# Kernel tuning notes

Measured on AMD Instinct MI355X. Metric: run time of the kernel, lower is better.

Reference implementation:

```python
import jax, jax.numpy as jnp
import numpy as np

PI = 3.141592653
PC_RANGE = np.array([-140.8, -40.0, -3.0, 140.8, 40.0, 1.0], np.float32)
IOU_THR = 0.1


def limit_period(val, offset=0.5, period=2 * PI):
    return val - jnp.floor(val / period + offset) * period


def pairwise_iou3d(boxes):
    # Axis-aligned 3D IoU approximation of the external boxes_iou3d_gpu CUDA kernel
    # (kernel source not provided). boxes: [N,7] = x,y,z,h,w,l,yaw; extents x<-l, y<-w, z<-h.
    c = boxes[:, :3]
    d = boxes[:, jnp.array([5, 4, 3])]
    lo = c - d * 0.5
    hi = c + d * 0.5
    inter = jnp.clip(jnp.minimum(hi[:, None, :], hi[None, :, :]) - jnp.maximum(lo[:, None, :], lo[None, :, :]), 0.0)
    inter_v = inter.prod(-1)                       # [N,N]
    vol = d.prod(-1)                               # [N]
    return inter_v / jnp.maximum(vol[:, None] + vol[None, :] - inter_v, 1e-8)


def cluster_assign(iou):
    # Greedy sequential clustering: repeatedly take the first unassigned box and
    # assign every box with iou > 0.1 (including already-assigned ones -> overwrite)
    # to a new cluster id. Equivalent to the original while-loop since an index,
    # once nonzero, never returns to zero, so the "first zero" scans left-to-right.
    iou = jax.lax.stop_gradient(iou)
    n = iou.shape[0]

    def body(i, carry):
        idx, cid = carry
        is_new = idx[i] == 0
        idx = jnp.where(is_new & (iou[i] > IOU_THR), cid, idx)
        return idx, cid + jnp.where(is_new, 1, 0).astype(jnp.int32)

    idx0 = jnp.zeros(n, jnp.int32)
    idx, cid = jax.lax.fori_loop(0, n, body, (idx0, jnp.int32(1)))
    return idx, cid


def cluster_fusion(boxes, scores, indices):
    n = boxes.shape[0]
    ids = jnp.arange(1, n + 1, dtype=jnp.int32)
    M = indices[None, :] == ids[:, None]            # [K,N] membership, K==N (padded)
    s_m = jnp.where(M, scores[None, :], 0.0)        # masked scores
    s_sum = s_m.sum(1)
    s_norm = s_m / jnp.maximum(s_sum, 1e-12)[:, None]
    dirs = boxes[:, 6]
    ref_idx = jnp.argmax(jnp.where(M, scores[None, :], -jnp.inf), axis=1)
    ref_dir = dirs[ref_idx]                         # yaw of max-score box per cluster
    diff = jnp.abs(dirs[None, :] - ref_dir[:, None])
    diff = jnp.where(diff > PI, 2 * PI - diff, diff)
    gt = diff > PI / 2
    score_gt = (s_m * gt).sum(1)
    score_le = s_sum - score_gt
    flip = jnp.where((score_gt <= score_le)[:, None], gt, ~gt)
    dirs_adj = limit_period(dirs[None, :] + PI * flip)
    theta = jnp.arctan2((jnp.sin(dirs_adj) * s_norm).sum(1), (jnp.cos(dirs_adj) * s_norm).sum(1))
    center_dim = s_norm @ boxes[:, :6]              # [K,6] score-weighted fusion
    boxes_fused = jnp.concatenate([center_dim, theta[:, None]], axis=1)
    # score fusion: sum_i s_sorted[i] ** (i+1), clipped to 1 (zeros from padding contribute 0)
    s_sorted = jnp.sort(s_m, axis=1)[:, ::-1]
    powers = jnp.arange(1, n + 1, dtype=jnp.float32)
    s_fused = jnp.minimum((s_sorted ** powers[None, :]).sum(1), 1.0)
    member = M.any(1)
    return boxes_fused, s_fused, member


def boxes_to_corners_3d(boxes):
    # order 'hwl': dims = h,w,l; l along x, w along y, h along z; rotate about z by yaw
    x, y, z = boxes[:, 0], boxes[:, 1], boxes[:, 2]
    h, w, l = boxes[:, 3], boxes[:, 4], boxes[:, 5]
    yaw = boxes[:, 6]
    xs = jnp.array([1, 1, -1, -1, 1, 1, -1, -1], jnp.float32) * 0.5
    ys = jnp.array([-1, 1, 1, -1, -1, 1, 1, -1], jnp.float32) * 0.5
    zs = jnp.array([-1, -1, -1, -1, 1, 1, 1, 1], jnp.float32) * 0.5
    cx = l[:, None] * xs
    cy = w[:, None] * ys
    cz = h[:, None] * zs
    c_, s_ = jnp.cos(yaw)[:, None], jnp.sin(yaw)[:, None]
    rx = cx * c_ - cy * s_
    ry = cx * s_ + cy * c_
    return jnp.stack([rx + x[:, None], ry + y[:, None], cz + z[:, None]], axis=-1)  # [N,8,3]


def setup_inputs() -> dict:
    key = jax.random.key(0)
    k1, k2, k3, k4, k5, k6 = jax.random.split(key, 6)
    C, M = 512, 8                # 512 objects seen by 8 agents -> 4096 detections
    N = C * M
    cx = jax.random.uniform(k1, (C,), minval=-120.0, maxval=120.0)
    cy = jax.random.uniform(k2, (C,), minval=-35.0, maxval=35.0)
    centers = jnp.stack([cx, cy, jnp.zeros(C)], -1)                     # [C,3]
    pos = (centers[:, None, :] + jax.random.normal(k3, (C, M, 3)) * 0.3).reshape(N, 3)
    dims = jnp.array([[1.56, 1.84, 4.2]]) + jax.random.normal(k4, (N, 3)) * 0.05  # h,w,l
    base_yaw = jax.random.uniform(k5, (C, 1), minval=-PI, maxval=PI)
    yaw = (base_yaw + jax.random.normal(k6, (C, M)) * 0.1).reshape(N, 1)
    boxes = jnp.concatenate([pos, dims, yaw], axis=1).astype(jnp.float32)
    scores = jax.random.uniform(jax.random.fold_in(key, 9), (N,), minval=0.05, maxval=0.95).astype(jnp.float32)
    return {"boxes": boxes, "scores": scores}


def reference(boxes, scores):
    boxes = boxes.at[:, 6].set(limit_period(boxes[:, 6]))
    iou = pairwise_iou3d(boxes)
    indices, _ = cluster_assign(iou)
    boxes_f, scores_f, member = cluster_fusion(boxes, scores, indices)
    corners = boxes_to_corners_3d(boxes_f)
    in_range = ((corners[..., 0] > PC_RANGE[0]) & (corners[..., 0] < PC_RANGE[3]) &
                (corners[..., 1] > PC_RANGE[1]) & (corners[..., 1] < PC_RANGE[4])).all(1)
    valid = member & in_range
    newid = jnp.cumsum(valid.astype(jnp.int32))     # remap surviving cluster ids to 1..K'
    safe = jnp.maximum(indices - 1, 0)
    new_indices = jnp.where((indices > 0) & valid[safe], newid[safe], 0)
    boxes_out = jnp.where(valid[:, None], boxes_f, 0.0)
    scores_out = jnp.where(valid, scores_f, 0.0)
    return boxes_out, scores_out, valid, new_indices
```

## Files before the change

### kernel.cpp

```cpp
#include <hip/hip_runtime.h>
#include <math.h>

#define PI_F      3.141592653f
#define TWO_PI_F  6.283185306f
#define HALF_PI_F 1.5707963265f
#define IOU_THR_F 0.1f

typedef unsigned long long u64;

__device__ __forceinline__ float limit_period_f(float v) {
    return v - floorf(v / TWO_PI_F + 0.5f) * TWO_PI_F;
}

__global__ void adj_kernel(const float* __restrict__ boxes,
                           u64* __restrict__ adjC,
                           unsigned char* __restrict__ occByte,
                           int n, int words) {
    __shared__ float jS[7][64];
    int w = blockIdx.x;
    int tid = threadIdx.x;
    int lane = tid & 63, wv = tid >> 6;
    if (tid < 64) {
        int j = (w << 6) + tid;
        if (j < n) {
            float b0 = boxes[j*7+0], b1 = boxes[j*7+1], b2 = boxes[j*7+2];
            float b3 = boxes[j*7+3], b4 = boxes[j*7+4], b5 = boxes[j*7+5];
            jS[0][tid] = b0 - b5*0.5f;  jS[3][tid] = b0 + b5*0.5f;
            jS[1][tid] = b1 - b4*0.5f;  jS[4][tid] = b1 + b4*0.5f;
            jS[2][tid] = b2 - b3*0.5f;  jS[5][tid] = b2 + b3*0.5f;
            jS[6][tid] = (b5*b4)*b3;
        }
    }
    __syncthreads();
    int i = blockIdx.y * 256 + tid;
    u64 word = 0ull;
    if (i < n) {
        float b0 = boxes[i*7+0], b1 = boxes[i*7+1], b2 = boxes[i*7+2];
        float b3 = boxes[i*7+3], b4 = boxes[i*7+4], b5 = boxes[i*7+5];
        float lix = b0 - b5*0.5f, hix = b0 + b5*0.5f;
        float liy = b1 - b4*0.5f, hiy = b1 + b4*0.5f;
        float liz = b2 - b3*0.5f, hiz = b2 + b3*0.5f;
        float vi  = (b5*b4)*b3;
        int jmax = n - (w << 6); if (jmax > 64) jmax = 64;
        for (int jj = 0; jj < jmax; ++jj) {
            float ix = fminf(hix, jS[3][jj]) - fmaxf(lix, jS[0][jj]); ix = fmaxf(ix, 0.0f);
            float iy = fminf(hiy, jS[4][jj]) - fmaxf(liy, jS[1][jj]); iy = fmaxf(iy, 0.0f);
            float iz = fminf(hiz, jS[5][jj]) - fmaxf(liz, jS[2][jj]); iz = fmaxf(iz, 0.0f);
            float inter = (ix*iy)*iz;
            float u = fmaxf(vi + jS[6][jj] - inter, 1e-8f);
            bool pred = (inter / u) > IOU_THR_F;
            word |= ((u64)(pred ? 1 : 0)) << jj;
        }
        adjC[(size_t)w * n + i] = word;
    }
    u64 bal = __ballot((i < n) && word != 0ull);
    int rb = blockIdx.y * 4 + wv;
    if (lane == 0 && rb < 64)
        occByte[rb * 64 + w] = bal ? (unsigned char)1 : (unsigned char)0;
}

__global__ __launch_bounds__(1024) void mis_node_kernel(
        const u64* __restrict__ adjC,
        const unsigned char* __restrict__ occByte,
        int* __restrict__ indices,
        int* __restrict__ seedList,
        int* __restrict__ nclust,
        int n, int words) {
    __shared__ u64 S_l[64], R_l[64], occL[64];
    __shared__ int unresolved;
    __shared__ int wsS[64];
    int tid = threadIdx.x;
    int lane = tid & 63, wv = tid >> 6;

    for (int rb = wv; rb < 64; rb += 16) {
        unsigned char b = occByte[rb * 64 + lane];
        u64 m = __ballot(b != 0);
        if (lane == 0) occL[rb] = m;
    }
    if (tid < 64) {
        int base = tid << 6;
        int vb = n - base;
        u64 valid = (vb >= 64) ? ~0ull : ((vb <= 0) ? 0ull : ((1ull << vb) - 1ull));
        S_l[tid] = 0ull;
        R_l[tid] = ~valid;
    }
    __syncthreads();

    u64 nzm[4];
    #pragma unroll
    for (int k = 0; k < 4; ++k) {
        int i = (k << 10) + tid;
        u64 nz = 0ull;
        if (i < n) {
            u64 oc = occL[i >> 6];
            while (oc) {
                int e = (int)__ffsll(oc) - 1; oc &= oc - 1;
                if (e < words && adjC[(size_t)e * n + i] != 0ull) nz |= 1ull << e;
            }
        }
        nzm[k] = nz;
    }

    unsigned done = 0;
    #pragma unroll
    for (int k = 0; k < 4; ++k)
        if (((k << 10) + tid) >= n) done |= 1u << k;

    for (;;) {
        if (tid == 0) unresolved = 0;
        unsigned pendSeed = 0, pendRes = 0;
        #pragma unroll
        for (int k = 0; k < 4; ++k) {
            if (done & (1u << k)) continue;
            int i = (k << 10) + tid;
            int w_i = i >> 6, b_i = i & 63;
            u64 sA = 0ull, uA = 0ull;
            u64 m = nzm[k];
            while (m) {
                int e = (int)__ffsll(m) - 1; m &= m - 1;
                if (e > w_i) break;
                u64 row = adjC[(size_t)e * n + i];
                u64 em = (e < w_i) ? ~0ull : (b_i ? ((1ull << b_i) - 1ull) : 0ull);
                sA |= row & S_l[e] & em;
                uA |= row & ~R_l[e] & em;
            }
            if (sA) pendRes |= 1u << k;
            else if (!uA) { pendSeed |= 1u << k; pendRes |= 1u << k; }
        }
        __syncthreads();
        #pragma unroll
        for (int k = 0; k < 4; ++k) {
            u64 bS = __ballot((pendSeed >> k) & 1u);
            u64 bR = __ballot((pendRes  >> k) & 1u);
            int w_i = ((k << 10) + tid) >> 6;
            if (lane == 0 && w_i < 64) {
                if (bS) atomicOr(&S_l[w_i], bS);
                if (bR) atomicOr(&R_l[w_i], bR);
            }
        }
        done |= pendRes;
        if ((done & 0xFu) != 0xFu) unresolved = 1;
        __syncthreads();
        if (unresolved == 0) break;
    }

    if (tid < 64) {
        int pc = (int)__popcll(S_l[tid]);
        int x = pc;
        for (int o = 1; o < 64; o <<= 1) {
            int y = __shfl_up(x, o);
            if (tid >= o) x += y;
        }
        wsS[tid] = x - pc;
        if (tid == 63) *nclust = x;
    }
    __syncthreads();
    #pragma unroll
    for (int k = 0; k < 4; ++k) {
        int i = (k << 10) + tid;
        if (i >= n) continue;
        int best = -1;
        u64 m = nzm[k];
        while (m) {
            int e = (int)__ffsll(m) - 1; m &= m - 1;
            u64 s = adjC[(size_t)e * n + i] & S_l[e];
            if (s) best = (e << 6) + 63 - (int)__clzll(s);
        }
        int idx = 0;
        if (best >= 0) {
            int w2 = best >> 6, b = best & 63;
            u64 incl = (b >= 63) ? ~0ull : ((2ull << b) - 1ull);
            idx = wsS[w2] + (int)__popcll(S_l[w2] & incl);
        }
        indices[i] = idx;
        int wj = i >> 6, bj = i & 63;
        if ((S_l[wj] >> bj) & 1ull) {
            int rank = wsS[wj] + (int)__popcll(S_l[wj] & (bj ? ((1ull << bj) - 1ull) : 0ull)) + 1;
            seedList[rank - 1] = i;
        }
    }
}

__global__ void fusion_kernel(const float* __restrict__ boxes,
                              const float* __restrict__ scores,
                              const int* __restrict__ indices,
                              const int* __restrict__ seedListG,
                              const int* __restrict__ nclust,
                              const u64* __restrict__ adjC,
                              float* __restrict__ fused,
                              float* __restrict__ sfused,
                              int* __restrict__ validArr, int n, int words) {
    int lane = threadIdx.x;
    int nc = *nclust;
    __shared__ unsigned short js[256];
    __shared__ float ms[256];
    __shared__ float ds[256];
    __shared__ float bx[6][256];
    __shared__ float sv[256], cv[256], pw[256];
    __shared__ float refdirS, denomS;
    __shared__ int   flipS, mS;
    for (int i = blockIdx.x; i < n; i += gridDim.x) {
        int cid = i + 1;
        if (cid > nc) {
            if (lane < 7) fused[i*7+lane] = 0.0f;
            if (lane == 0) { sfused[i] = 0.0f; validArr[i] = 0; }
            continue;
        }
        int s = seedListG[i];
        u64 bits = (lane < words) ? adjC[(size_t)lane * n + s] : 0ull;
        u64 keep = 0ull;
        u64 t = bits;
        while (t) {
            int b = (int)__ffsll(t) - 1;
            t &= t - 1;
            int node = (lane << 6) + b;
            if (indices[node] == cid) keep |= (1ull << b);
        }
        int cnt = __popcll(keep);
        int x = cnt;
        for (int o = 1; o < 64; o <<= 1) {
            int y = __shfl_up(x, o);
            if (lane >= o) x += y;
        }
        int excl = x - cnt;
        int m = __shfl(x, 63);
        int pos = excl;
        t = keep;
        while (t) {
            int b = (int)__ffsll(t) - 1;
            t &= t - 1;
            js[pos++] = (unsigned short)((lane << 6) + b);
        }
        __syncthreads();
        for (int k = lane; k < m; k += 64) {
            int j = js[k];
            ms[k] = scores[j];
            ds[k] = limit_period_f(boxes[j*7+6]);
            bx[0][k] = boxes[j*7+0];
            bx[1][k] = boxes[j*7+1];
            bx[2][k] = boxes[j*7+2];
            bx[3][k] = boxes[j*7+3];
            bx[4][k] = boxes[j*7+4];
            bx[5][k] = boxes[j*7+5];
        }
        __syncthreads();
        if (m == 0) {
            if (lane == 0) {
                for (int k = 0; k < 7; ++k) fused[i*7+k] = 0.0f;
                sfused[i] = 0.0f; validArr[i] = 0;
            }
            __syncthreads();
            continue;
        }
        if (lane == 0) {
            float ssum = 0.0f, smax = -1e30f; int kref = 0;
            for (int k = 0; k < m; ++k) {
                float sc = ms[k];
                ssum += sc;
                if (sc > smax) { smax = sc; kref = k; }
            }
            float refdir = ds[kref];
            float denom = fmaxf(ssum, 1e-12f);
            float sgt = 0.0f;
            for (int k = 0; k < m; ++k) {
                float d = fabsf(ds[k] - refdir);
                if (d > PI_F) d = TWO_PI_F - d;
                if (d > HALF_PI_F) sgt += ms[k];
            }
            float sle = ssum - sgt;
            refdirS = refdir; denomS = denom;
            flipS = (sgt <= sle) ? 1 : 0;
        }
        __syncthreads();
        {
            float refdir = refdirS, denom = denomS;
            bool flipGt = flipS != 0;
            for (int k = lane; k < m; k += 64) {
                float dj = ds[k];
                float d = fabsf(dj - refdir);
                if (d > PI_F) d = TWO_PI_F - d;
                bool gt = d > HALF_PI_F;
                bool flip = flipGt ? gt : !gt;
                float adj_d = limit_period_f(dj + (flip ? PI_F : 0.0f));
                float wgt = ms[k] / denom;
                sv[k] = sinf(adj_d) * wgt;
                cv[k] = cosf(adj_d) * wgt;
            }
        }
        __syncthreads();
        if (lane == 0) {
            float refdir = refdirS, denom = denomS;
            float sgt_dummy = 0.0f; (void)sgt_dummy; (void)refdir;
            float cd0=0,cd1=0,cd2=0,cd3=0,cd4=0,cd5=0;
            for (int k = 0; k < m; ++k) {
                float wgt = ms[k] / denom;
                cd0 += wgt * bx[0][k];
                cd1 += wgt * bx[1][k];
                cd2 += wgt * bx[2][k];
                cd3 += wgt * bx[3][k];
                cd4 += wgt * bx[4][k];
                cd5 += wgt * bx[5][k];
            }
            float ssin = 0.0f, scos = 0.0f;
            for (int k = 0; k < m; ++k) { ssin += sv[k]; scos += cv[k]; }
            float theta = atan2f(ssin, scos);
            for (int k = 1; k < m; ++k) {
                float key = ms[k]; int p = k - 1;
                while (p >= 0 && ms[p] < key) { ms[p+1] = ms[p]; --p; }
                ms[p+1] = key;
            }
            bx[0][255] = cd0; bx[1][255] = cd1; bx[2][255] = cd2;
            bx[3][255] = cd3; bx[4][255] = cd4; bx[5][255] = cd5;
            sv[255] = theta;
            mS = m;
        }
        __syncthreads();
        for (int k = lane; k < m; k += 64)
            pw[k] = powf(ms[k], (float)(k+1));
        __syncthreads();
        if (lane == 0) {
            float cd0 = bx[0][255], cd1 = bx[1][255], cd2 = bx[2][255];
            float cd3 = bx[3][255], cd4 = bx[4][255], cd5 = bx[5][255];
            float theta = sv[255];
            float sf = 0.0f;
            for (int k = 0; k < m; ++k) sf += pw[k];
            sf = fminf(sf, 1.0f);
            float c_ = cosf(theta), s_ = sinf(theta);
            float wdim = cd4, ldim = cd5;
            const float xs[4]  = {0.5f, 0.5f, -0.5f, -0.5f};
            const float ys_[4] = {-0.5f, 0.5f, 0.5f, -0.5f};
            bool inr = true;
            for (int c = 0; c < 4; ++c) {
                float cx = ldim * xs[c], cy = wdim * ys_[c];
                float rx = cx*c_ - cy*s_ + cd0;
                float ry = cx*s_ + cy*c_ + cd1;
                inr = inr && (rx > -140.8f) && (rx < 140.8f) && (ry > -40.0f) && (ry < 40.0f);
            }
            fused[i*7+0]=cd0; fused[i*7+1]=cd1; fused[i*7+2]=cd2;
            fused[i*7+3]=cd3; fused[i*7+4]=cd4; fused[i*7+5]=cd5;
            fused[i*7+6]=theta;
            sfused[i] = sf;
            validArr[i] = inr ? 1 : 0;
        }
        __syncthreads();
    }
}

__global__ void finalize_kernel(const float* __restrict__ fused,
                                const float* __restrict__ sfused,
                                const int* __restrict__ validArr,
                                const int* __restrict__ indices,
                                float* __restrict__ out, int n) {
    __shared__ int newidS[4096];
    __shared__ unsigned char validS[4096];
    __shared__ int scanBuf[1024];
    int tid = threadIdx.x;
    int per = (n + 1023) >> 10;
    int base = tid * per;
    int v[8];
    int sum = 0;
    for (int k = 0; k < per && k < 8; ++k) {
        int j = base + k;
        int vv = (j < n) ? validArr[j] : 0;
        v[k] = vv; sum += vv;
    }
    scanBuf[tid] = sum;
    __syncthreads();
    for (int o = 1; o < 1024; o <<= 1) {
        int val = scanBuf[tid];
        int add = (tid >= o) ? scanBuf[tid - o] : 0;
        __syncthreads();
        scanBuf[tid] = val + add;
        __syncthreads();
    }
    int run = scanBuf[tid] - sum;
    for (int k = 0; k < per && k < 8; ++k) {
        int j = base + k;
        if (j < n) { run += v[k]; newidS[j] = run; validS[j] = (unsigned char)v[k]; }
    }
    __syncthreads();
    float* boxesO  = out;
    float* scoresO = out + (size_t)7*n;
    float* validO  = out + (size_t)8*n;
    float* idxO    = out + (size_t)9*n;
    for (int j = tid; j < n; j += 1024) {
        int vv = validS[j];
        #pragma unroll
        for (int k = 0; k < 7; ++k)
            boxesO[j*7+k] = vv ? fused[j*7+k] : 0.0f;
        scoresO[j] = vv ? sfused[j] : 0.0f;
        validO[j]  = vv ? 1.0f : 0.0f;
        int ind = indices[j];
        int safe = ind - 1; if (safe < 0) safe = 0;
        bool nv = (ind > 0) && (validS[safe] != 0);
        idxO[j] = nv ? (float)newidS[safe] : 0.0f;
    }
}

extern "C" void kernel_launch(void* const* d_in, const int* in_sizes, int n_in,
                              void* d_out, int out_size, void* d_ws, size_t ws_size,
                              hipStream_t stream) {
    const float* boxes  = (const float*)d_in[0];
    const float* scores = (const float*)d_in[1];
    int n = in_sizes[0] / 7;
    int words = (n + 63) >> 6;

    char* ws = (char*)d_ws;
    size_t off = 0;
    u64* adjC = (u64*)(ws + off);
    off += (size_t)n * words * sizeof(u64);
    unsigned char* occByte = (unsigned char*)(ws + off); off += 64 * 64;
    int* seedList = (int*)(ws + off); off += (size_t)n * sizeof(int);
    int* indices  = (int*)(ws + off); off += (size_t)n * sizeof(int);
    float* fused  = (float*)(ws + off); off += (size_t)n * 7 * sizeof(float);
    float* sfused = (float*)(ws + off); off += (size_t)n * sizeof(float);
    int* validArr = (int*)(ws + off); off += (size_t)n * sizeof(int);
    int* nclust   = (int*)(ws + off); off += sizeof(int);

    dim3 adjGrid(words, (n + 255) / 256);
    adj_kernel<<<adjGrid, 256, 0, stream>>>(boxes, adjC, occByte, n, words);
    mis_node_kernel<<<1, 1024, 0, stream>>>(adjC, occByte, indices, seedList,
                                            nclust, n, words);
    fusion_kernel<<<512, 64, 0, stream>>>(boxes, scores, indices, seedList, nclust,
                                          adjC, fused, sfused, validArr, n, words);
    finalize_kernel<<<1, 1024, 0, stream>>>(fused, sfused, validArr, indices,
                                            (float*)d_out, n);
}
```

Measured before the change: 94.51 us.

## Cache neighbor rows in registers and move index assignment into fusion kernel

The single-block MIS kernel now caches up to four nonzero lower-triangle adjacency words per node in registers, with an overflow mask for the rest. This avoids reloading them from global memory on every resolution round. Thread-to-node mapping changes so each wave covers one 64-node row block. The per-node cluster index assignment moves out of the serial one-block kernel into the 512-block fusion kernel, which computes indices only for candidate members of each seed. Indices are zero-initialized in the adjacency kernel, and the seed list is built per word by scanning bits. The trade-off is more register pressure, capped 320-candidate buffers that could truncate large clusters, and redundant per-cluster index computation.

```diff
diff --git a/kernel.cpp b/kernel.cpp
--- a/kernel.cpp
+++ b/kernel.cpp
@@ -15,11 +15,16 @@
 __global__ void adj_kernel(const float* __restrict__ boxes,
                            u64* __restrict__ adjC,
                            unsigned char* __restrict__ occByte,
+                           int* __restrict__ indices,
                            int n, int words) {
     __shared__ float jS[7][64];
     int w = blockIdx.x;
     int tid = threadIdx.x;
     int lane = tid & 63, wv = tid >> 6;
+    if (blockIdx.x == 0) {
+        int i2 = blockIdx.y * 256 + tid;
+        if (i2 < n) indices[i2] = 0;
+    }
     if (tid < 64) {
         int j = (w << 6) + tid;
         if (j < n) {
@@ -59,12 +64,11 @@
         occByte[rb * 64 + w] = bal ? (unsigned char)1 : (unsigned char)0;
 }
 
-__global__ __launch_bounds__(1024) void mis_node_kernel(
+__global__ __launch_bounds__(1024) void mis_round_kernel(
         const u64* __restrict__ adjC,
         const unsigned char* __restrict__ occByte,
-        int* __restrict__ indices,
-        int* __restrict__ seedList,
-        int* __restrict__ nclust,
+        u64* __restrict__ SG, u64* __restrict__ occLG,
+        int* __restrict__ seedList, int* __restrict__ nclust,
         int n, int words) {
     __shared__ u64 S_l[64], R_l[64], occL[64];
     __shared__ int unresolved;
@@ -85,26 +89,40 @@
         R_l[tid] = ~valid;
     }
     __syncthreads();
-
-    u64 nzm[4];
+    if (tid < 64) occLG[tid] = occL[tid];
+
+    int id0[4], id1[4], id2[4], id3[4];
+    u64 r0[4], r1[4], r2[4], r3[4], rstR[4];
     #pragma unroll
     for (int k = 0; k < 4; ++k) {
-        int i = (k << 10) + tid;
-        u64 nz = 0ull;
-        if (i < n) {
-            u64 oc = occL[i >> 6];
-            while (oc) {
-                int e = (int)__ffsll(oc) - 1; oc &= oc - 1;
-                if (e < words && adjC[(size_t)e * n + i] != 0ull) nz |= 1ull << e;
-            }
-        }
-        nzm[k] = nz;
+        int rb = (k << 4) + wv;
+        int i = (rb << 6) + lane;
+        id0[k] = id1[k] = id2[k] = id3[k] = 0xFF;
+        r0[k] = r1[k] = r2[k] = r3[k] = 0ull; rstR[k] = 0ull;
+        u64 lowm = lane ? ((1ull << lane) - 1ull) : 0ull;
+        u64 oc = occL[rb] & ((rb >= 63) ? ~0ull : ((2ull << rb) - 1ull));
+        int cnt = 0;
+        while (oc) {
+            int e = (int)__ffsll(oc) - 1; oc &= oc - 1;
+            if (e >= words) break;
+            u64 row = (i < n) ? adjC[(size_t)e * n + i] : 0ull;
+            u64 em = (e < rb) ? ~0ull : lowm;
+            u64 re = row & em;
+            if (re) {
+                if      (cnt == 0) { id0[k] = e; r0[k] = re; }
+                else if (cnt == 1) { id1[k] = e; r1[k] = re; }
+                else if (cnt == 2) { id2[k] = e; r2[k] = re; }
+                else if (cnt == 3) { id3[k] = e; r3[k] = re; }
+                else rstR[k] |= 1ull << e;
+                ++cnt;
+            }
+        }
     }
 
     unsigned done = 0;
     #pragma unroll
     for (int k = 0; k < 4; ++k)
-        if (((k << 10) + tid) >= n) done |= 1u << k;
+        if ((((k << 4) + wv) << 6) + lane >= n) done |= 1u << k;
 
     for (;;) {
         if (tid == 0) unresolved = 0;
@@ -112,15 +130,19 @@
         #pragma unroll
         for (int k = 0; k < 4; ++k) {
             if (done & (1u << k)) continue;
-            int i = (k << 10) + tid;
-            int w_i = i >> 6, b_i = i & 63;
+            int rb = (k << 4) + wv;
+            int i = (rb << 6) + lane;
+            u64 lowm = lane ? ((1ull << lane) - 1ull) : 0ull;
             u64 sA = 0ull, uA = 0ull;
-            u64 m = nzm[k];
-            while (m) {
-                int e = (int)__ffsll(m) - 1; m &= m - 1;
-                if (e > w_i) break;
+            if (id0[k] != 0xFF) { sA |= r0[k] & S_l[id0[k]]; uA |= r0[k] & ~R_l[id0[k]]; }
+            if (id1[k] != 0xFF) { sA |= r1[k] & S_l[id1[k]]; uA |= r1[k] & ~R_l[id1[k]]; }
+            if (id2[k] != 0xFF) { sA |= r2[k] & S_l[id2[k]]; uA |= r2[k] & ~R_l[id2[k]]; }
+            if (id3[k] != 0xFF) { sA |= r3[k] & S_l[id3[k]]; uA |= r3[k] & ~R_l[id3[k]]; }
+            u64 rm = rstR[k];
+            while (rm) {
+                int e = (int)__ffsll(rm) - 1; rm &= rm - 1;
                 u64 row = adjC[(size_t)e * n + i];
-                u64 em = (e < w_i) ? ~0ull : (b_i ? ((1ull << b_i) - 1ull) : 0ull);
+                u64 em = (e < rb) ? ~0ull : lowm;
                 sA |= row & S_l[e] & em;
                 uA |= row & ~R_l[e] & em;
             }
@@ -132,10 +154,10 @@
         for (int k = 0; k < 4; ++k) {
             u64 bS = __ballot((pendSeed >> k) & 1u);
             u64 bR = __ballot((pendRes  >> k) & 1u);
-            int w_i = ((k << 10) + tid) >> 6;
-            if (lane == 0 && w_i < 64) {
-                if (bS) atomicOr(&S_l[w_i], bS);
-                if (bR) atomicOr(&R_l[w_i], bR);
+            int rb = (k << 4) + wv;
+            if (lane == 0 && rb < 64) {
+                if (bS) atomicOr(&S_l[rb], bS);
+                if (bR) atomicOr(&R_l[rb], bR);
             }
         }
         done |= pendRes;
@@ -145,7 +167,9 @@
     }
 
     if (tid < 64) {
-        int pc = (int)__popcll(S_l[tid]);
+        u64 s = S_l[tid];
+        SG[tid] = s;
+        int pc = (int)__popcll(s);
         int x = pc;
         for (int o = 1; o < 64; o <<= 1) {
             int y = __shfl_up(x, o);
@@ -155,50 +179,53 @@
         if (tid == 63) *nclust = x;
     }
     __syncthreads();
-    #pragma unroll
-    for (int k = 0; k < 4; ++k) {
-        int i = (k << 10) + tid;
-        if (i >= n) continue;
-        int best = -1;
-        u64 m = nzm[k];
-        while (m) {
-            int e = (int)__ffsll(m) - 1; m &= m - 1;
-            u64 s = adjC[(size_t)e * n + i] & S_l[e];
-            if (s) best = (e << 6) + 63 - (int)__clzll(s);
-        }
-        int idx = 0;
-        if (best >= 0) {
-            int w2 = best >> 6, b = best & 63;
-            u64 incl = (b >= 63) ? ~0ull : ((2ull << b) - 1ull);
-            idx = wsS[w2] + (int)__popcll(S_l[w2] & incl);
-        }
-        indices[i] = idx;
-        int wj = i >> 6, bj = i & 63;
-        if ((S_l[wj] >> bj) & 1ull) {
-            int rank = wsS[wj] + (int)__popcll(S_l[wj] & (bj ? ((1ull << bj) - 1ull) : 0ull)) + 1;
-            seedList[rank - 1] = i;
+    if (tid < 64) {
+        u64 sbits = S_l[tid];
+        int r = wsS[tid];
+        while (sbits) {
+            int b = (int)__ffsll(sbits) - 1; sbits &= sbits - 1;
+            seedList[r++] = (tid << 6) + b;
         }
     }
 }
 
 __global__ void fusion_kernel(const float* __restrict__ boxes,
                               const float* __restrict__ scores,
-                              const int* __restrict__ indices,
+                              const u64* __restrict__ SG,
+                              const u64* __restrict__ occLG,
                               const int* __restrict__ seedListG,
                               const int* __restrict__ nclust,
                               const u64* __restrict__ adjC,
+                              int* __restrict__ indices,
                               float* __restrict__ fused,
                               float* __restrict__ sfused,
                               int* __restrict__ validArr, int n, int words) {
     int lane = threadIdx.x;
-    int nc = *nclust;
-    __shared__ unsigned short js[256];
+    __shared__ u64 S_s[64];
+    __shared__ int ws_s[64];
+    __shared__ u64 occ_s[64];
+    __shared__ unsigned short js[320], js2[320];
+    __shared__ unsigned char keepB[320];
     __shared__ float ms[256];
     __shared__ float ds[256];
     __shared__ float bx[6][256];
     __shared__ float sv[256], cv[256], pw[256];
     __shared__ float refdirS, denomS;
-    __shared__ int   flipS, mS;
+    __shared__ int   flipS;
+    {
+        u64 s = (lane < words) ? SG[lane] : 0ull;
+        S_s[lane] = s;
+        occ_s[lane] = occLG[lane];
+        int pc = (int)__popcll(s);
+        int x = pc;
+        for (int o = 1; o < 64; o <<= 1) {
+            int y = __shfl_up(x, o);
+            if (lane >= o) x += y;
+        }
+        ws_s[lane] = x - pc;
+    }
+    __syncthreads();
+    int nc = *nclust;
     for (int i = blockIdx.x; i < n; i += gridDim.x) {
         int cid = i + 1;
         if (cid > nc) {
@@ -208,32 +235,60 @@
         }
         int s = seedListG[i];
         u64 bits = (lane < words) ? adjC[(size_t)lane * n + s] : 0ull;
-        u64 keep = 0ull;
+        int cnt = __popcll(bits);
+        int x = cnt;
+        for (int o = 1; o < 64; o <<= 1) {
+            int y = __shfl_up(x, o);
+            if (lane >= o) x += y;
+        }
+        int excl = x - cnt;
+        int mc = __shfl(x, 63);
+        if (mc > 320) mc = 320;
+        int pos = excl;
         u64 t = bits;
         while (t) {
             int b = (int)__ffsll(t) - 1;
             t &= t - 1;
-            int node = (lane << 6) + b;
-            if (indices[node] == cid) keep |= (1ull << b);
-        }
-        int cnt = __popcll(keep);
-        int x = cnt;
-        for (int o = 1; o < 64; o <<= 1) {
-            int y = __shfl_up(x, o);
-            if (lane >= o) x += y;
-        }
-        int excl = x - cnt;
-        int m = __shfl(x, 63);
-        int pos = excl;
-        t = keep;
-        while (t) {
-            int b = (int)__ffsll(t) - 1;
-            t &= t - 1;
-            js[pos++] = (unsigned short)((lane << 6) + b);
+            if (pos < 320) js[pos] = (unsigned short)((lane << 6) + b);
+            ++pos;
+        }
+        __syncthreads();
+        for (int k = lane; k < mc; k += 64) {
+            int j = js[k];
+            int rb = j >> 6;
+            int best = -1;
+            u64 oc = occ_s[rb];
+            while (oc) {
+                int e = 63 - (int)__clzll(oc); oc &= ~(1ull << e);
+                if (e >= words) continue;
+                u64 m2 = adjC[(size_t)e * n + j] & S_s[e];
+                if (m2) { best = (e << 6) + 63 - (int)__clzll(m2); break; }
+            }
+            int idx = 0;
+            if (best >= 0) {
+                int w2 = best >> 6, b = best & 63;
+                u64 incl = (b >= 63) ? ~0ull : ((2ull << b) - 1ull);
+                idx = ws_s[w2] + (int)__popcll(S_s[w2] & incl);
+            }
+            bool kp = (idx == cid);
+            keepB[k] = kp ? 1 : 0;
+            if (kp) indices[j] = idx;
+        }
+        __syncthreads();
+        int m = 0;
+        for (int base2 = 0; base2 < mc; base2 += 64) {
+            int kk = base2 + lane;
+            bool kp = (kk < mc) && keepB[kk];
+            u64 bal = __ballot(kp);
+            if (kp) {
+                int p2 = m + (int)__popcll(bal & ((1ull << lane) - 1ull));
+                if (p2 < 320) js2[p2] = js[kk];
+            }
+            m += (int)__popcll(bal);
         }
         __syncthreads();
         for (int k = lane; k < m; k += 64) {
-            int j = js[k];
+            int j = js2[k];
             ms[k] = scores[j];
             ds[k] = limit_period_f(boxes[j*7+6]);
             bx[0][k] = boxes[j*7+0];
@@ -289,8 +344,7 @@
         }
         __syncthreads();
         if (lane == 0) {
-            float refdir = refdirS, denom = denomS;
-            float sgt_dummy = 0.0f; (void)sgt_dummy; (void)refdir;
+            float denom = denomS;
             float cd0=0,cd1=0,cd2=0,cd3=0,cd4=0,cd5=0;
             for (int k = 0; k < m; ++k) {
                 float wgt = ms[k] / denom;
@@ -312,7 +366,6 @@
             bx[0][255] = cd0; bx[1][255] = cd1; bx[2][255] = cd2;
             bx[3][255] = cd3; bx[4][255] = cd4; bx[5][255] = cd5;
             sv[255] = theta;
-            mS = m;
         }
         __syncthreads();
         for (int k = lane; k < m; k += 64)
@@ -410,6 +463,8 @@
     u64* adjC = (u64*)(ws + off);
     off += (size_t)n * words * sizeof(u64);
     unsigned char* occByte = (unsigned char*)(ws + off); off += 64 * 64;
+    u64* SG     = (u64*)(ws + off); off += 64 * sizeof(u64);
+    u64* occLG  = (u64*)(ws + off); off += 64 * sizeof(u64);
     int* seedList = (int*)(ws + off); off += (size_t)n * sizeof(int);
     int* indices  = (int*)(ws + off); off += (size_t)n * sizeof(int);
     float* fused  = (float*)(ws + off); off += (size_t)n * 7 * sizeof(float);
@@ -418,11 +473,12 @@
     int* nclust   = (int*)(ws + off); off += sizeof(int);
 
     dim3 adjGrid(words, (n + 255) / 256);
-    adj_kernel<<<adjGrid, 256, 0, stream>>>(boxes, adjC, occByte, n, words);
-    mis_node_kernel<<<1, 1024, 0, stream>>>(adjC, occByte, indices, seedList,
-                                            nclust, n, words);
-    fusion_kernel<<<512, 64, 0, stream>>>(boxes, scores, indices, seedList, nclust,
-                                          adjC, fused, sfused, validArr, n, words);
+    adj_kernel<<<adjGrid, 256, 0, stream>>>(boxes, adjC, occByte, indices, n, words);
+    mis_round_kernel<<<1, 1024, 0, stream>>>(adjC, occByte, SG, occLG, seedList,
+                                             nclust, n, words);
+    fusion_kernel<<<512, 64, 0, stream>>>(boxes, scores, SG, occLG, seedList, nclust,
+                                          adjC, indices, fused, sfused, validArr,
+                                          n, words);
     finalize_kernel<<<1, 1024, 0, stream>>>(fused, sfused, validArr, indices,
                                             (float*)d_out, n);
 }
```

Measured after the change: 91.70 us. 3.0% less time.
